# Performance work log

Measured on AMD Instinct MI355X. Metric: run time of the kernel, lower is better.

The kernel has to match this reference:

```python
import jax, jax.numpy as jnp
import numpy as np
import math

G = 8; N0 = 16384; DEG = 8; E = G * N0 * DEG
C = 128; H = 256; OUT = 128; L = 3
RATIO = 0.5; EPS_FA = 0.1


def setup_inputs():
    key = jax.random.key(0)
    ks = jax.random.split(key, 10)
    x = jax.random.normal(ks[0], (G * N0, C), jnp.float32)
    e = jax.random.randint(ks[1], (2, E), 0, N0)
    off = jnp.repeat(jnp.arange(G) * N0, N0 * DEG)  # per-graph node offsets
    edge_index = (e + off[None, :]).astype(jnp.int32)  # (2, E), edges stay within their graph
    batch = jnp.repeat(jnp.arange(G), N0).astype(jnp.int32)
    root = jax.random.normal(ks[2], (G, C), jnp.float32)
    s = 0.05
    att_l = jax.random.normal(ks[3], (L, C), jnp.float32) * s
    att_r = jax.random.normal(ks[4], (L, C), jnp.float32) * s
    w_ih = jax.random.normal(ks[5], (3 * H, C * L), jnp.float32) * s
    w_hh = jax.random.normal(ks[6], (3 * H, H), jnp.float32) * s
    b_ih = jnp.zeros(3 * H, jnp.float32)
    b_hh = jnp.zeros(3 * H, jnp.float32)
    w_fin = jax.random.normal(ks[7], (OUT, H), jnp.float32) * s
    b_fin = jnp.zeros(OUT, jnp.float32)
    w_root = jax.random.normal(ks[8], (OUT, C), jnp.float32) * s
    b_root = jnp.zeros(OUT, jnp.float32)
    residual_alpha = jnp.float32(0.5)
    return dict(x=x, edge_index=edge_index, batch=batch, root=root, att_l=att_l, att_r=att_r,
                w_ih=w_ih, w_hh=w_hh, b_ih=b_ih, b_hh=b_hh, w_fin=w_fin, b_fin=b_fin,
                w_root=w_root, b_root=b_root, residual_alpha=residual_alpha)


def _faconv(xc, x0, src, dst, emask, al_w, ar_w, n):
    # gcn_norm with self-loops: deg over dst (+1 for self loop), w_ij = d_i^-1/2 d_j^-1/2
    deg = jax.ops.segment_sum(emask, dst, num_segments=n) + 1.0
    dinv = jax.lax.rsqrt(deg)
    w = dinv[src] * dinv[dst] * emask
    al = xc @ al_w  # (n,)
    ar = xc @ ar_w
    alpha = jnp.tanh(al[dst] + ar[src])
    out = jax.ops.segment_sum((w * alpha)[:, None] * xc[src], dst, num_segments=n)
    # self-loop message (weight 1/deg_i, alpha = tanh(al_i + ar_i))
    out = out + ((dinv * dinv) * jnp.tanh(al + ar))[:, None] * xc
    return out + EPS_FA * x0


def _forward(x, root, att_l, att_r, w_ih, w_hh, b_ih, b_hh, w_fin, b_fin, w_root, b_root, residual_alpha, edge_index):
    src = edge_index[0]
    dst = edge_index[1]
    emask = jnp.ones(src.shape[0], jnp.float32)  # edge validity mask (replaces dynamic edge filtering)
    cur, orig = x, x
    npg = N0  # nodes per graph at current layer (static)
    outs = []
    for i in range(L):
        n = G * npg
        h = jax.nn.relu(_faconv(cur, orig, src, dst, emask, att_l[i], att_r[i], n))
        outs.append(h.reshape(G, npg, C).max(axis=1))  # global_max_pool per graph
        # ASTGPool: score = out-degree on edge_index[0], per-graph top-k (k = ceil(npg*ratio))
        score = jax.ops.segment_sum(emask, src, num_segments=n)
        k = int(math.ceil(npg * RATIO))
        _, idx = jax.lax.top_k(score.reshape(G, npg), k)
        perm = (idx + (jnp.arange(G) * npg)[:, None]).reshape(-1)  # (G*k,) global kept-node ids
        keep = jnp.zeros(n, bool).at[perm].set(True)
        emask = emask * keep[src].astype(jnp.float32) * keep[dst].astype(jnp.float32)
        nmap = jnp.zeros(n, src.dtype).at[perm].set(jnp.arange(G * k, dtype=src.dtype))
        src, dst = nmap[src], nmap[dst]  # dead edges map to node 0 but have emask==0
        cur, orig, npg = h[perm], orig[perm], k  # multiplier = 1.0
    fused = jnp.concatenate(outs, axis=1)  # (G, C*L)
    # single-step GRU with h0 = 0
    gi = fused @ w_ih.T + b_ih
    ir, iz, inn = jnp.split(gi, 3, axis=1)
    br, bz, bn = jnp.split(b_hh, 3)
    r = jax.nn.sigmoid(ir + br)
    z = jax.nn.sigmoid(iz + bz)
    ncand = jnp.tanh(inn + r * bn)
    hgru = (1.0 - z) * ncand
    gnn_emb = hgru @ w_fin.T + b_fin
    root_emb = root @ w_root.T + b_root
    return residual_alpha * gnn_emb + (1.0 - residual_alpha) * root_emb


def reference(x, edge_index, batch, root, att_l, att_r, w_ih, w_hh, b_ih, b_hh, w_fin, b_fin, w_root, b_root, residual_alpha):
    del batch  # graphs are contiguous equal-size blocks; batch structure is encoded in G, N0
    return _forward(x, root, att_l, att_r, w_ih, w_hh, b_ih, b_hh, w_fin, b_fin, w_root, b_root, residual_alpha, edge_index)
```

## Files before the change

kernel.cpp:

```cpp
#include <hip/hip_runtime.h>
#include <math.h>

#define G 8
#define N0 16384
#define NEDGE (G*N0*8)
#define EPG (NEDGE/G)
#define C 128
#define EPS_FA 0.1f
#define SMAX 2048

typedef unsigned short ushort_t;
typedef unsigned int uint_t;

__device__ inline ushort_t f2bf(float f) {
    uint_t u = __float_as_uint(f);
    uint_t r = (u + 0x7FFFu + ((u >> 16) & 1u)) >> 16;
    return (ushort_t)r;
}
__device__ inline uint_t pack2bf(float a, float b) {
    return (uint_t)f2bf(a) | ((uint_t)f2bf(b) << 16);
}
__device__ inline float bflo(uint_t w) { return __uint_as_float(w << 16); }
__device__ inline float bfhi(uint_t w) { return __uint_as_float(w & 0xFFFF0000u); }

__global__ void __launch_bounds__(256) k_hist0(const int* __restrict__ ei,
                                               unsigned int* __restrict__ bh,
                                               ushort_t* __restrict__ lrank) {
    __shared__ unsigned int h[N0];
    int t = threadIdx.x;
    for (int i = t; i < N0; i += 256) h[i] = 0;
    __syncthreads();
    int base = blockIdx.x * 8192;
    int gbase = (blockIdx.x >> 4) * N0;
    for (int i = t; i < 8192; i += 256) {
        int s = ei[base + i] - gbase;
        int d = ei[NEDGE + base + i] - gbase;
        unsigned int old = atomicAdd(&h[d], 1u);
        lrank[base + i] = (ushort_t)(old & 0xFFFFu);
        atomicAdd(&h[s], 0x10000u);
    }
    __syncthreads();
    unsigned int* o = bh + (size_t)blockIdx.x * N0;
    for (int i = t; i < N0; i += 256) o[i] = h[i];
}

__global__ void k_sumdeg(unsigned int* __restrict__ bh, int* __restrict__ degI,
                         int* __restrict__ score, int shift, int nsub, int n,
                         float* __restrict__ pooled) {
    int i = blockIdx.x * 256 + threadIdx.x;
    if (pooled && i < G * 384) pooled[i] = 0.0f;
    if (i >= n) return;
    int bins = 1 << shift;
    int g = i >> shift, u = i & (bins - 1);
    unsigned int* p = bh + ((size_t)(g * nsub) << shift) + u;
    unsigned int run = 0; int as = 0;
    for (int b = 0; b < nsub; b++) {
        unsigned int w = p[(size_t)b * bins];
        p[(size_t)b * bins] = run;
        run += w & 0xFFFFu; as += (int)(w >> 16);
    }
    degI[i] = (int)run; score[i] = as;
}

__global__ void k_alar(const float* __restrict__ x,
                       const float* __restrict__ attl, const float* __restrict__ attr,
                       float* __restrict__ al, float* __restrict__ ar,
                       ushort_t* __restrict__ xb, int n) {
    int wid  = (blockIdx.x * blockDim.x + threadIdx.x) >> 6;
    int lane = threadIdx.x & 63;
    if (wid >= n) return;
    float2 v  = ((const float2*)(x + (size_t)wid * C))[lane];
    ((uint_t*)(xb + (size_t)wid * C))[lane] = pack2bf(v.x, v.y);
    float2 l2 = ((const float2*)attl)[lane];
    float2 r2 = ((const float2*)attr)[lane];
    float sl = v.x * l2.x + v.y * l2.y;
    float sr = v.x * r2.x + v.y * r2.y;
    for (int o = 32; o >= 1; o >>= 1) { sl += __shfl_xor(sl, o); sr += __shfl_xor(sr, o); }
    if (lane == 0) { al[wid] = sl; ar[wid] = sr; }
}

__global__ void __launch_bounds__(256) k_scan1(const int* __restrict__ degI,
                                               int* __restrict__ rowptr,
                                               int* __restrict__ bsum) {
    __shared__ int part[256];
    int t = threadIdx.x;
    int base = blockIdx.x * 2048 + t * 8;
    int v[8]; int s = 0;
    for (int i = 0; i < 8; i++) { v[i] = degI[base + i]; s += v[i]; }
    part[t] = s; __syncthreads();
    for (int o = 1; o < 256; o <<= 1) {
        int val = part[t];
        int add = (t >= o) ? part[t - o] : 0;
        __syncthreads();
        part[t] = val + add;
        __syncthreads();
    }
    int run = (t == 0) ? 0 : part[t - 1];
    if (t == 255) bsum[blockIdx.x] = part[255];
    for (int i = 0; i < 8; i++) { rowptr[base + i] = run; run += v[i]; }
}

__global__ void k_scan3s(int* __restrict__ rowptr,
                         const int* __restrict__ bsum, const int* __restrict__ degI,
                         const float* __restrict__ al, const float* __restrict__ ar,
                         float* __restrict__ dinv, float* __restrict__ selfco,
                         unsigned char* __restrict__ keep, int* __restrict__ nmap, int n) {
    __shared__ int base_s;
    int t = threadIdx.x;
    if (t < 64) {
        int c = blockIdx.x >> 3;
        int vv = (t < c) ? bsum[t] : 0;
        for (int o = 32; o >= 1; o >>= 1) vv += __shfl_xor(vv, o);
        if (t == 0) base_s = vv;
    }
    __syncthreads();
    int i = blockIdx.x * 256 + t;
    if (i >= n) return;
    rowptr[i] += base_s;
    float d  = (float)degI[i] + 1.0f;
    float di = rsqrtf(d);
    dinv[i]   = di;
    selfco[i] = di * di * tanhf(al[i] + ar[i]);
    keep[i] = 0; nmap[i] = 0;
}

__global__ void k_fill(const int* __restrict__ src, const int* __restrict__ dst,
                       const unsigned char* __restrict__ em,
                       const float* __restrict__ dinv, const float* __restrict__ al,
                       const float* __restrict__ ar,
                       const int* __restrict__ rowptr,
                       const unsigned int* __restrict__ bpre,
                       const ushort_t* __restrict__ lrank,
                       int2* __restrict__ edges,
                       int ebShift, int nsubShift, int binShift) {
    int gph = blockIdx.x & 7;
    int chunk = blockIdx.x >> 3;
    int e = gph * EPG + chunk * 256 + threadIdx.x;
    if (em && !em[e]) return;
    int s = src[e], d = dst[e];
    float cf = dinv[s] * dinv[d] * tanhf(al[d] + ar[s]);
    int b = e >> ebShift;
    int gb = (b >> nsubShift) << binShift;
    int slot = rowptr[d] + (int)bpre[((size_t)b << binShift) + (d - gb)] + (int)lrank[e];
    edges[slot] = make_int2(s, __float_as_int(cf));
}

#define ACC4(W, CF) { a0 += (CF) * bflo((W).x); a1 += (CF) * bfhi((W).x); \
                      a2 += (CF) * bflo((W).y); a3 += (CF) * bfhi((W).y); }
__global__ void __launch_bounds__(256) k_msg_csr(
        const int* __restrict__ rowptr, const int* __restrict__ degI,
        const int2* __restrict__ edges,
        const ushort_t* __restrict__ cur, const ushort_t* __restrict__ xb,
        const int* __restrict__ oidx, const float* __restrict__ selfco,
        ushort_t* __restrict__ h, float* __restrict__ pb, int npg) {
    __shared__ float pm[8 * 128];
    int g    = blockIdx.x & 7;
    int ib   = blockIdx.x >> 3;
    int sub  = threadIdx.x >> 5;
    int lane = threadIdx.x & 31;
    int v = g * npg + ib * 8 + sub;
    int rs = rowptr[v], deg = degI[v];
    int o = oidx ? oidx[v] : v;
    uint2 cw = ((const uint2*)(cur + (size_t)v * C))[lane];
    uint2 xw = ((const uint2*)(xb  + (size_t)o * C))[lane];
    float sc = selfco[v];
    float a0 = 0.0f, a1 = 0.0f, a2 = 0.0f, a3 = 0.0f;
    for (int j0 = 0; j0 < deg; j0 += 32) {
        int cnt = deg - j0; if (cnt > 32) cnt = 32;
        int2 er = make_int2(0, 0);
        if (lane < cnt) er = edges[rs + j0 + lane];
        uint2 w0 = make_uint2(0,0), w1 = w0, w2 = w0, w3 = w0;
        {
            int s0 = __shfl(er.x, 0, 32);
            if (0 < cnt) w0 = ((const uint2*)(cur + (size_t)s0 * C))[lane];
            int s1 = __shfl(er.x, 1, 32);
            if (1 < cnt) w1 = ((const uint2*)(cur + (size_t)s1 * C))[lane];
            int s2 = __shfl(er.x, 2, 32);
            if (2 < cnt) w2 = ((const uint2*)(cur + (size_t)s2 * C))[lane];
            int s3 = __shfl(er.x, 3, 32);
            if (3 < cnt) w3 = ((const uint2*)(cur + (size_t)s3 * C))[lane];
        }
        int j = 0;
        for (; j + 4 <= cnt; j += 4) {
            float cf0 = __int_as_float(__shfl(er.y, j, 32));
            ACC4(w0, cf0);
            int sn0 = __shfl(er.x, j + 4, 32);
            if (j + 4 < cnt) w0 = ((const uint2*)(cur + (size_t)sn0 * C))[lane];
            float cf1 = __int_as_float(__shfl(er.y, j + 1, 32));
            ACC4(w1, cf1);
            int sn1 = __shfl(er.x, j + 5, 32);
            if (j + 5 < cnt) w1 = ((const uint2*)(cur + (size_t)sn1 * C))[lane];
            float cf2 = __int_as_float(__shfl(er.y, j + 2, 32));
            ACC4(w2, cf2);
            int sn2 = __shfl(er.x, j + 6, 32);
            if (j + 6 < cnt) w2 = ((const uint2*)(cur + (size_t)sn2 * C))[lane];
            float cf3 = __int_as_float(__shfl(er.y, j + 3, 32));
            ACC4(w3, cf3);
            int sn3 = __shfl(er.x, j + 7, 32);
            if (j + 7 < cnt) w3 = ((const uint2*)(cur + (size_t)sn3 * C))[lane];
        }
        if (j < cnt)     { float cf = __int_as_float(__shfl(er.y, j,     32)); ACC4(w0, cf); }
        if (j + 1 < cnt) { float cf = __int_as_float(__shfl(er.y, j + 1, 32)); ACC4(w1, cf); }
        if (j + 2 < cnt) { float cf = __int_as_float(__shfl(er.y, j + 2, 32)); ACC4(w2, cf); }
    }
    float r0 = fmaxf(a0 + sc * bflo(cw.x) + EPS_FA * bflo(xw.x), 0.0f);
    float r1 = fmaxf(a1 + sc * bfhi(cw.x) + EPS_FA * bfhi(xw.x), 0.0f);
    float r2 = fmaxf(a2 + sc * bflo(cw.y) + EPS_FA * bflo(xw.y), 0.0f);
    float r3 = fmaxf(a3 + sc * bfhi(cw.y) + EPS_FA * bfhi(xw.y), 0.0f);
    uint2 hw; hw.x = pack2bf(r0, r1); hw.y = pack2bf(r2, r3);
    ((uint2*)(h + (size_t)v * C))[lane] = hw;
    float4 rr = make_float4(r0, r1, r2, r3);
    ((float4*)(pm + sub * 128))[lane] = rr;
    __syncthreads();
    int t = threadIdx.x;
    if (t < 128) {
        float m = pm[t];
        for (int s = 1; s < 8; s++) m = fmaxf(m, pm[s * 128 + t]);
        pb[(size_t)blockIdx.x * 128 + t] = m;
    }
}

__global__ void __launch_bounds__(256) k_poolred(const float* __restrict__ pb,
                                                 float* __restrict__ pooled, int layer) {
    __shared__ float sm[256];
    int g = blockIdx.x & 7;
    int ch = blockIdx.x >> 3;
    int t = threadIdx.x;
    int c = t & 127, half = t >> 7;
    float m = 0.0f;
    for (int i = 0; i < 32; i++) {
        int r = ch * 64 + half * 32 + i;
        m = fmaxf(m, pb[(size_t)(g + 8 * r) * 128 + c]);
    }
    sm[t] = m;
    __syncthreads();
    if (t < 128) {
        float mm = fmaxf(sm[t], sm[t + 128]);
        atomicMax((unsigned int*)&pooled[g * 384 + layer * 128 + c], __float_as_uint(mm));
    }
}

__global__ void __launch_bounds__(256) k_hist(const int* __restrict__ score, int npg, int nb,
                                              int* __restrict__ blockhist) {
    __shared__ int lh[SMAX];
    int g = blockIdx.x / nb, b = blockIdx.x % nb, t = threadIdx.x;
    for (int s = t; s < SMAX; s += 256) lh[s] = 0;
    __syncthreads();
    int s = score[g * npg + b * 256 + t];
    if (s > SMAX - 1) s = SMAX - 1;
    atomicAdd(&lh[s], 1);
    __syncthreads();
    int* outp = blockhist + ((size_t)g * nb + b) * SMAX;
    for (int i = t; i < SMAX; i += 256) outp[i] = lh[i];
}

__global__ void __launch_bounds__(256) k_binprefix(int* __restrict__ blockhist,
                                                   int* __restrict__ hist, int nb) {
    __shared__ int tile[64 * 256];
    int g = blockIdx.x >> 3, ch = blockIdx.x & 7, t = threadIdx.x;
    int s0 = ch * 256;
    int* bg = blockhist + (size_t)g * nb * SMAX + s0;
    for (int b = 0; b < nb; b++) tile[b * 256 + t] = bg[(size_t)b * SMAX + t];
    __syncthreads();
    int acc = 0;
    for (int b = 0; b < nb; b++) {
        int v = tile[b * 256 + t];
        tile[b * 256 + t] = acc;
        acc += v;
    }
    __syncthreads();
    for (int b = 0; b < nb; b++) bg[(size_t)b * SMAX + t] = tile[b * 256 + t];
    hist[g * SMAX + s0 + t] = acc;
}

__global__ void __launch_bounds__(256) k_rank(const int* __restrict__ score,
                                              const int* __restrict__ blockhist,
                                              const int* __restrict__ hist,
                                              int npg, int nb, int k,
                                              unsigned char* __restrict__ keep,
                                              int* __restrict__ nmap, int* __restrict__ perm) {
    __shared__ int bp[SMAX];
    __shared__ int part[256];
    __shared__ int cs[256];
    int g = blockIdx.x / nb, b = blockIdx.x % nb, t = threadIdx.x;
    const int* hg = hist + g * SMAX;
    int v[8]; int sm = 0;
    for (int i = 0; i < 8; i++) { v[i] = hg[SMAX - 1 - (t * 8 + i)]; sm += v[i]; }
    part[t] = sm; __syncthreads();
    for (int o = 1; o < 256; o <<= 1) {
        int val = part[t];
        int add = (t >= o) ? part[t - o] : 0;
        __syncthreads();
        part[t] = val + add;
        __syncthreads();
    }
    int run = (t == 0) ? 0 : part[t - 1];
    for (int i = 0; i < 8; i++) { bp[SMAX - 1 - (t * 8 + i)] = run; run += v[i]; }
    int vv = b * 256 + t;
    int s = score[g * npg + vv];
    if (s > SMAX - 1) s = SMAX - 1;
    cs[t] = s;
    __syncthreads();
    int cnt = 0;
    for (int u = 0; u < t; u++) cnt += (cs[u] == s);
    int pos = bp[s] + blockhist[((size_t)g * nb + b) * SMAX + s] + cnt;
    if (pos < k) {
        int vg = g * npg + vv;
        int nid = g * k + pos;
        keep[vg] = 1; nmap[vg] = nid; perm[nid] = vg;
    }
}

__global__ void k_gather_alar(const ushort_t* __restrict__ h, const int* __restrict__ perm,
                              const int* __restrict__ oidx,
                              const float* __restrict__ attlN, const float* __restrict__ attrN,
                              ushort_t* __restrict__ curN, int* __restrict__ oidxN,
                              float* __restrict__ al, float* __restrict__ ar, int m) {
    int i = blockIdx.x * 256 + threadIdx.x;
    if (i >= m * 32) return;
    int j = i >> 5, c4 = i & 31;
    int p = perm[j];
    uint2 w = ((const uint2*)(h + (size_t)p * C))[c4];
    ((uint2*)(curN + (size_t)j * C))[c4] = w;
    float f0 = bflo(w.x), f1 = bfhi(w.x), f2 = bflo(w.y), f3 = bfhi(w.y);
    float4 l4 = ((const float4*)attlN)[c4];
    float4 r4 = ((const float4*)attrN)[c4];
    float sl = f0 * l4.x + f1 * l4.y + f2 * l4.z + f3 * l4.w;
    float sr = f0 * r4.x + f1 * r4.y + f2 * r4.z + f3 * r4.w;
    for (int o = 16; o >= 1; o >>= 1) { sl += __shfl_xor(sl, o); sr += __shfl_xor(sr, o); }
    if (c4 == 0) {
        al[j] = sl; ar[j] = sr;
        oidxN[j] = oidx ? oidx[p] : p;
    }
}

__global__ void __launch_bounds__(256) k_remap_hist(
        const int* __restrict__ inS, const int* __restrict__ inD,
        const unsigned char* __restrict__ inEm,
        int* __restrict__ src, int* __restrict__ dst, unsigned char* __restrict__ em,
        const unsigned char* __restrict__ keep, const int* __restrict__ nmap,
        unsigned int* __restrict__ bh, ushort_t* __restrict__ lrank, int kN) {
    __shared__ unsigned int h[8192];
    int t = threadIdx.x;
    for (int i = t; i < kN; i += 256) h[i] = 0;
    __syncthreads();
    int base = blockIdx.x * 4096;
    int gb = (blockIdx.x >> 5) * kN;
    for (int i = t; i < 4096; i += 256) {
        int e = base + i;
        int s = inS[e], d = inD[e];
        bool ok = (!inEm || inEm[e]) && keep[s] && keep[d];
        if (ok) {
            int ns = nmap[s], nd = nmap[d];
            src[e] = ns; dst[e] = nd; em[e] = 1;
            unsigned int old = atomicAdd(&h[nd - gb], 1u);
            lrank[e] = (ushort_t)(old & 0xFFFFu);
            atomicAdd(&h[ns - gb], 0x10000u);
        } else { src[e] = 0; dst[e] = 0; em[e] = 0; }
    }
    __syncthreads();
    unsigned int* o = bh + (size_t)blockIdx.x * kN;
    for (int i = t; i < kN; i += 256) o[i] = h[i];
}

__global__ void __launch_bounds__(256) k_gi(const float* __restrict__ pooled,
                                            const float* __restrict__ wih,
                                            const float* __restrict__ bih,
                                            float* __restrict__ gi) {
    int g = blockIdx.y;
    int row = blockIdx.x * 4 + (threadIdx.x >> 6);
    int lane = threadIdx.x & 63;
    const float* w = wih + (size_t)row * 384;
    const float* f = pooled + g * 384;
    float s = 0.0f;
    #pragma unroll
    for (int i = 0; i < 6; i++) s += w[i * 64 + lane] * f[i * 64 + lane];
    for (int o = 32; o >= 1; o >>= 1) s += __shfl_xor(s, o);
    if (lane == 0) gi[g * 768 + row] = s + bih[row];
}

__global__ void __launch_bounds__(256) k_gru_fin(const float* __restrict__ gi,
        const float* __restrict__ bhh, const float* __restrict__ wfin,
        const float* __restrict__ bfin, const float* __restrict__ wroot,
        const float* __restrict__ broot, const float* __restrict__ rootv,
        const float* __restrict__ alphap, float* __restrict__ out) {
    int g = blockIdx.x, t = threadIdx.x;
    __shared__ float hg[256];
    {
        float r  = 1.0f / (1.0f + expf(-(gi[g * 768 + t]       + bhh[t])));
        float z  = 1.0f / (1.0f + expf(-(gi[g * 768 + 256 + t] + bhh[256 + t])));
        float nc = tanhf(gi[g * 768 + 512 + t] + r * bhh[512 + t]);
        hg[t] = (1.0f - z) * nc;
    }
    __syncthreads();
    float a = alphap[0];
    int wv = t >> 6, lane = t & 63;
    const float* rg = rootv + (size_t)g * 128;
    for (int oo = 0; oo < 32; oo++) {
        int o = wv * 32 + oo;
        const float* wf = wfin + (size_t)o * 256;
        float sf = wf[lane] * hg[lane] + wf[64 + lane] * hg[64 + lane]
                 + wf[128 + lane] * hg[128 + lane] + wf[192 + lane] * hg[192 + lane];
        const float* wr = wroot + (size_t)o * 128;
        float sr = wr[lane] * rg[lane] + wr[64 + lane] * rg[64 + lane];
        float s = a * sf + (1.0f - a) * sr;
        for (int sh = 32; sh >= 1; sh >>= 1) s += __shfl_xor(s, sh);
        if (lane == 0)
            out[g * 128 + o] = s + a * bfin[o] + (1.0f - a) * broot[o];
    }
}

extern "C" void kernel_launch(void* const* d_in, const int* in_sizes, int n_in,
                              void* d_out, int out_size, void* d_ws, size_t ws_size,
                              hipStream_t stream) {
    const float* x      = (const float*)d_in[0];
    const int*   ei     = (const int*)d_in[1];
    const float* rootv  = (const float*)d_in[3];
    const float* att_l  = (const float*)d_in[4];
    const float* att_r  = (const float*)d_in[5];
    const float* w_ih   = (const float*)d_in[6];
    const float* b_ih   = (const float*)d_in[8];
    const float* b_hh   = (const float*)d_in[9];
    const float* w_fin  = (const float*)d_in[10];
    const float* b_fin  = (const float*)d_in[11];
    const float* w_root = (const float*)d_in[12];
    const float* b_root = (const float*)d_in[13];
    const float* alphap = (const float*)d_in[14];
    float* out = (float*)d_out;

    char* wsb = (char*)d_ws;
    size_t off = 0;
    auto alloc = [&](size_t bytes) -> char* {
        char* p = wsb + off; off += (bytes + 255) & ~(size_t)255; return p;
    };
    ushort_t* xb   = (ushort_t*)alloc((size_t)131072 * C * 2);
    ushort_t* bufH = (ushort_t*)alloc((size_t)131072 * C * 2);
    ushort_t* bufC = (ushort_t*)alloc((size_t)65536  * C * 2);
    int*   srcA   = (int*)alloc((size_t)NEDGE * 4);
    int*   dstA   = (int*)alloc((size_t)NEDGE * 4);
    unsigned char* emask = (unsigned char*)alloc(NEDGE);
    int2*  edges  = (int2*)alloc((size_t)NEDGE * 8);
    ushort_t* lrank = (ushort_t*)alloc((size_t)NEDGE * 2);
    float* al     = (float*)alloc(131072 * 4);
    float* ar     = (float*)alloc(131072 * 4);
    float* dinv   = (float*)alloc(131072 * 4);
    float* selfco = (float*)alloc(131072 * 4);
    int*   degI   = (int*)alloc(131072 * 4);
    int*   score  = (int*)alloc(131072 * 4);
    int*   rowptr = (int*)alloc(131072 * 4);
    int*   bsum   = (int*)alloc(256 * 4);
    unsigned char* keep = (unsigned char*)alloc(131072);
    int*   nmap   = (int*)alloc(131072 * 4);
    int*   perm   = (int*)alloc(65536 * 4);
    int*   oidxA  = (int*)alloc(65536 * 4);
    int*   oidxB  = (int*)alloc(32768 * 4);
    float* pooled = (float*)alloc(G * 384 * 4);
    float* giBuf  = (float*)alloc(G * 768 * 4);
    int*   blockhist = (int*)alloc((size_t)G * 64 * SMAX * 4);
    int*   histT  = (int*)alloc((size_t)G * SMAX * 4);
    unsigned int* bh = (unsigned int*)alloc((size_t)128 * N0 * 4);
    float* pb = (float*)bh;

    k_hist0<<<128, 256, 0, stream>>>(ei, bh, lrank);
    k_sumdeg<<<131072 / 256, 256, 0, stream>>>(bh, degI, score, 14, 16, 131072, pooled);

    const int ns[3]   = {131072, 65536, 32768};
    const int npgs[3] = {16384, 8192, 4096};
    const int ks[3]   = {8192, 4096, 0};
    const int shifts[3] = {14, 13, 12};

    for (int l = 0; l < 3; l++) {
        int n = ns[l], npg = npgs[l], k = ks[l];
        const ushort_t* cur = (l == 0) ? xb : bufC;
        const int* oidx = (l == 0) ? nullptr : (l == 1 ? oidxA : oidxB);
        int* oidxN = (l == 0) ? oidxA : oidxB;
        const int* eS = (l == 0) ? ei : srcA;
        const int* eD = (l == 0) ? ei + NEDGE : dstA;
        const unsigned char* eM = (l == 0) ? nullptr : emask;
        int ebShift   = (l == 0) ? 13 : 12;
        int nsubShift = (l == 0) ? 4  : 5;
        int binShift  = shifts[l];

        if (l == 0)
            k_alar<<<n / 4, 256, 0, stream>>>(x, att_l, att_r, al, ar, xb, n);

        int nblk = n / 2048;
        k_scan1<<<nblk, 256, 0, stream>>>(degI, rowptr, bsum);
        k_scan3s<<<n / 256, 256, 0, stream>>>(rowptr, bsum, degI, al, ar,
                                              dinv, selfco, keep, nmap, n);

        k_fill<<<NEDGE / 256, 256, 0, stream>>>(eS, eD, eM, dinv, al, ar,
                                                rowptr, bh, lrank, edges,
                                                ebShift, nsubShift, binShift);
        k_msg_csr<<<n / 8, 256, 0, stream>>>(rowptr, degI, edges, cur, xb, oidx,
                                             selfco, bufH, pb, npg);
        k_poolred<<<npg / 64, 256, 0, stream>>>(pb, pooled, l);

        if (l < 2) {
            int nb = npg / 256;
            k_hist<<<G * nb, 256, 0, stream>>>(score, npg, nb, blockhist);
            k_binprefix<<<G * 8, 256, 0, stream>>>(blockhist, histT, nb);
            k_rank<<<G * nb, 256, 0, stream>>>(score, blockhist, histT, npg, nb, k,
                                               keep, nmap, perm);
            int m = G * k;
            k_gather_alar<<<(m * 32 + 255) / 256, 256, 0, stream>>>(
                bufH, perm, oidx, att_l + (l + 1) * C, att_r + (l + 1) * C,
                bufC, oidxN, al, ar, m);
            k_remap_hist<<<256, 256, 0, stream>>>(eS, eD, eM, srcA, dstA, emask,
                                                  keep, nmap, bh, lrank, k);
            k_sumdeg<<<(G * k + 255) / 256, 256, 0, stream>>>(bh, degI, score,
                                                              shifts[l + 1], 32, G * k,
                                                              nullptr);
        }
    }

    k_gi<<<dim3(192, G), 256, 0, stream>>>(pooled, w_ih, b_ih, giBuf);
    k_gru_fin<<<G, 256, 0, stream>>>(giBuf, b_hh, w_fin, b_fin, w_root, b_root,
                                     rootv, alphap, out);
}
```

Before: 438.9 us.

## Merge independent kernels into combined launches to cut launch count

Pairs independent kernels that previously ran back to back: sumdeg with alar, fill with score histogram, message passing with bin prefix, pool reduction with rank, and gather with edge remap. Each combined launch splits its blocks by blockIdx range into the two roles. This removes several kernel launches and serialisation bubbles per layer, letting small kernels overlap with larger ones. The bin-prefix role is also retiled from 8 chunks of 256 to 32 chunks of 64, and merging raises shared-memory use in the combined kernels, which may lower occupancy for the heavy message kernel.

```diff
diff --git a/kernel.cpp b/kernel.cpp
--- a/kernel.cpp
+++ b/kernel.cpp
@@ -44,11 +44,41 @@
     for (int i = t; i < N0; i += 256) o[i] = h[i];
 }
 
+__global__ void __launch_bounds__(256) k_sumdeg_alar(
+        unsigned int* __restrict__ bh, int* __restrict__ degI, int* __restrict__ score,
+        float* __restrict__ pooled,
+        const float* __restrict__ x, const float* __restrict__ attl,
+        const float* __restrict__ attr, float* __restrict__ al, float* __restrict__ ar,
+        ushort_t* __restrict__ xb) {
+    int t = threadIdx.x;
+    if ((int)blockIdx.x < 512) {
+        int i = blockIdx.x * 256 + t;
+        if (i < G * 384) pooled[i] = 0.0f;
+        unsigned int* p = bh + ((size_t)((i >> 14) * 16) << 14) + (i & 16383);
+        unsigned int run = 0; int as = 0;
+        for (int b = 0; b < 16; b++) {
+            unsigned int w = p[(size_t)b << 14];
+            p[(size_t)b << 14] = run;
+            run += w & 0xFFFFu; as += (int)(w >> 16);
+        }
+        degI[i] = (int)run; score[i] = as;
+    } else {
+        int idx = (blockIdx.x - 512) * 256 + t;
+        int wid = idx >> 6, lane = idx & 63;
+        float2 v  = ((const float2*)(x + (size_t)wid * C))[lane];
+        ((uint_t*)(xb + (size_t)wid * C))[lane] = pack2bf(v.x, v.y);
+        float2 l2 = ((const float2*)attl)[lane];
+        float2 r2 = ((const float2*)attr)[lane];
+        float sl = v.x * l2.x + v.y * l2.y;
+        float sr = v.x * r2.x + v.y * r2.y;
+        for (int o = 32; o >= 1; o >>= 1) { sl += __shfl_xor(sl, o); sr += __shfl_xor(sr, o); }
+        if (lane == 0) { al[wid] = sl; ar[wid] = sr; }
+    }
+}
+
 __global__ void k_sumdeg(unsigned int* __restrict__ bh, int* __restrict__ degI,
-                         int* __restrict__ score, int shift, int nsub, int n,
-                         float* __restrict__ pooled) {
+                         int* __restrict__ score, int shift, int nsub, int n) {
     int i = blockIdx.x * 256 + threadIdx.x;
-    if (pooled && i < G * 384) pooled[i] = 0.0f;
     if (i >= n) return;
     int bins = 1 << shift;
     int g = i >> shift, u = i & (bins - 1);
@@ -62,23 +92,6 @@
     degI[i] = (int)run; score[i] = as;
 }
 
-__global__ void k_alar(const float* __restrict__ x,
-                       const float* __restrict__ attl, const float* __restrict__ attr,
-                       float* __restrict__ al, float* __restrict__ ar,
-                       ushort_t* __restrict__ xb, int n) {
-    int wid  = (blockIdx.x * blockDim.x + threadIdx.x) >> 6;
-    int lane = threadIdx.x & 63;
-    if (wid >= n) return;
-    float2 v  = ((const float2*)(x + (size_t)wid * C))[lane];
-    ((uint_t*)(xb + (size_t)wid * C))[lane] = pack2bf(v.x, v.y);
-    float2 l2 = ((const float2*)attl)[lane];
-    float2 r2 = ((const float2*)attr)[lane];
-    float sl = v.x * l2.x + v.y * l2.y;
-    float sr = v.x * r2.x + v.y * r2.y;
-    for (int o = 32; o >= 1; o >>= 1) { sl += __shfl_xor(sl, o); sr += __shfl_xor(sr, o); }
-    if (lane == 0) { al[wid] = sl; ar[wid] = sr; }
-}
-
 __global__ void __launch_bounds__(256) k_scan1(const int* __restrict__ degI,
                                                int* __restrict__ rowptr,
                                                int* __restrict__ bsum) {
@@ -124,40 +137,80 @@
     keep[i] = 0; nmap[i] = 0;
 }
 
-__global__ void k_fill(const int* __restrict__ src, const int* __restrict__ dst,
-                       const unsigned char* __restrict__ em,
-                       const float* __restrict__ dinv, const float* __restrict__ al,
-                       const float* __restrict__ ar,
-                       const int* __restrict__ rowptr,
-                       const unsigned int* __restrict__ bpre,
-                       const ushort_t* __restrict__ lrank,
-                       int2* __restrict__ edges,
-                       int ebShift, int nsubShift, int binShift) {
-    int gph = blockIdx.x & 7;
-    int chunk = blockIdx.x >> 3;
-    int e = gph * EPG + chunk * 256 + threadIdx.x;
-    if (em && !em[e]) return;
-    int s = src[e], d = dst[e];
-    float cf = dinv[s] * dinv[d] * tanhf(al[d] + ar[s]);
-    int b = e >> ebShift;
-    int gb = (b >> nsubShift) << binShift;
-    int slot = rowptr[d] + (int)bpre[((size_t)b << binShift) + (d - gb)] + (int)lrank[e];
-    edges[slot] = make_int2(s, __float_as_int(cf));
+__global__ void __launch_bounds__(256) k_fill_hist(
+        const int* __restrict__ src, const int* __restrict__ dst,
+        const unsigned char* __restrict__ em,
+        const float* __restrict__ dinv, const float* __restrict__ al,
+        const float* __restrict__ ar,
+        const int* __restrict__ rowptr, const unsigned int* __restrict__ bpre,
+        const ushort_t* __restrict__ lrank, int2* __restrict__ edges,
+        int ebShift, int nsubShift, int binShift,
+        const int* __restrict__ score, int npg, int nb,
+        int* __restrict__ blockhist, int histBlocks) {
+    __shared__ int lh[SMAX];
+    int t = threadIdx.x;
+    if ((int)blockIdx.x < histBlocks) {
+        int g = blockIdx.x / nb, b = blockIdx.x % nb;
+        for (int s = t; s < SMAX; s += 256) lh[s] = 0;
+        __syncthreads();
+        int s = score[g * npg + b * 256 + t];
+        if (s > SMAX - 1) s = SMAX - 1;
+        atomicAdd(&lh[s], 1);
+        __syncthreads();
+        int* outp = blockhist + ((size_t)g * nb + b) * SMAX;
+        for (int i = t; i < SMAX; i += 256) outp[i] = lh[i];
+    } else {
+        int fb = blockIdx.x - histBlocks;
+        int gph = fb & 7, chunk = fb >> 3;
+        int e = gph * EPG + chunk * 256 + t;
+        if (em && !em[e]) return;
+        int s = src[e], d = dst[e];
+        float cf = dinv[s] * dinv[d] * tanhf(al[d] + ar[s]);
+        int b = e >> ebShift;
+        int gb = (b >> nsubShift) << binShift;
+        int slot = rowptr[d] + (int)bpre[((size_t)b << binShift) + (d - gb)] + (int)lrank[e];
+        edges[slot] = make_int2(s, __float_as_int(cf));
+    }
 }
 
 #define ACC4(W, CF) { a0 += (CF) * bflo((W).x); a1 += (CF) * bfhi((W).x); \
                       a2 += (CF) * bflo((W).y); a3 += (CF) * bfhi((W).y); }
-__global__ void __launch_bounds__(256) k_msg_csr(
+__global__ void __launch_bounds__(256) k_msg_bp(
         const int* __restrict__ rowptr, const int* __restrict__ degI,
         const int2* __restrict__ edges,
         const ushort_t* __restrict__ cur, const ushort_t* __restrict__ xb,
         const int* __restrict__ oidx, const float* __restrict__ selfco,
-        ushort_t* __restrict__ h, float* __restrict__ pb, int npg) {
+        ushort_t* __restrict__ h, float* __restrict__ pb, int npg,
+        int* __restrict__ blockhist, int* __restrict__ histT, int nb, int bpBlocks) {
     __shared__ float pm[8 * 128];
-    int g    = blockIdx.x & 7;
-    int ib   = blockIdx.x >> 3;
-    int sub  = threadIdx.x >> 5;
-    int lane = threadIdx.x & 31;
+    __shared__ int tile[4096];
+    int t = threadIdx.x;
+    if ((int)blockIdx.x < bpBlocks) {
+        int g = blockIdx.x >> 5, ch = blockIdx.x & 31;
+        int s0 = ch * 64;
+        int* bg = blockhist + (size_t)g * nb * SMAX;
+        int tot = nb * 64;
+        for (int i = t; i < tot; i += 256)
+            tile[i] = bg[(size_t)(i >> 6) * SMAX + s0 + (i & 63)];
+        __syncthreads();
+        if (t < 64) {
+            int acc = 0;
+            for (int b = 0; b < nb; b++) {
+                int idx = b * 64 + t;
+                int v = tile[idx]; tile[idx] = acc; acc += v;
+            }
+            histT[g * SMAX + s0 + t] = acc;
+        }
+        __syncthreads();
+        for (int i = t; i < tot; i += 256)
+            bg[(size_t)(i >> 6) * SMAX + s0 + (i & 63)] = tile[i];
+        return;
+    }
+    int mb   = blockIdx.x - bpBlocks;
+    int g    = mb & 7;
+    int ib   = mb >> 3;
+    int sub  = t >> 5;
+    int lane = t & 31;
     int v = g * npg + ib * 8 + sub;
     int rs = rowptr[v], deg = degI[v];
     int o = oidx ? oidx[v] : v;
@@ -212,155 +265,120 @@
     float4 rr = make_float4(r0, r1, r2, r3);
     ((float4*)(pm + sub * 128))[lane] = rr;
     __syncthreads();
-    int t = threadIdx.x;
     if (t < 128) {
         float m = pm[t];
         for (int s = 1; s < 8; s++) m = fmaxf(m, pm[s * 128 + t]);
-        pb[(size_t)blockIdx.x * 128 + t] = m;
-    }
-}
-
-__global__ void __launch_bounds__(256) k_poolred(const float* __restrict__ pb,
-                                                 float* __restrict__ pooled, int layer) {
-    __shared__ float sm[256];
-    int g = blockIdx.x & 7;
-    int ch = blockIdx.x >> 3;
-    int t = threadIdx.x;
-    int c = t & 127, half = t >> 7;
-    float m = 0.0f;
-    for (int i = 0; i < 32; i++) {
-        int r = ch * 64 + half * 32 + i;
-        m = fmaxf(m, pb[(size_t)(g + 8 * r) * 128 + c]);
-    }
-    sm[t] = m;
-    __syncthreads();
-    if (t < 128) {
-        float mm = fmaxf(sm[t], sm[t + 128]);
-        atomicMax((unsigned int*)&pooled[g * 384 + layer * 128 + c], __float_as_uint(mm));
-    }
-}
-
-__global__ void __launch_bounds__(256) k_hist(const int* __restrict__ score, int npg, int nb,
-                                              int* __restrict__ blockhist) {
-    __shared__ int lh[SMAX];
-    int g = blockIdx.x / nb, b = blockIdx.x % nb, t = threadIdx.x;
-    for (int s = t; s < SMAX; s += 256) lh[s] = 0;
-    __syncthreads();
-    int s = score[g * npg + b * 256 + t];
-    if (s > SMAX - 1) s = SMAX - 1;
-    atomicAdd(&lh[s], 1);
-    __syncthreads();
-    int* outp = blockhist + ((size_t)g * nb + b) * SMAX;
-    for (int i = t; i < SMAX; i += 256) outp[i] = lh[i];
-}
-
-__global__ void __launch_bounds__(256) k_binprefix(int* __restrict__ blockhist,
-                                                   int* __restrict__ hist, int nb) {
-    __shared__ int tile[64 * 256];
-    int g = blockIdx.x >> 3, ch = blockIdx.x & 7, t = threadIdx.x;
-    int s0 = ch * 256;
-    int* bg = blockhist + (size_t)g * nb * SMAX + s0;
-    for (int b = 0; b < nb; b++) tile[b * 256 + t] = bg[(size_t)b * SMAX + t];
-    __syncthreads();
-    int acc = 0;
-    for (int b = 0; b < nb; b++) {
-        int v = tile[b * 256 + t];
-        tile[b * 256 + t] = acc;
-        acc += v;
-    }
-    __syncthreads();
-    for (int b = 0; b < nb; b++) bg[(size_t)b * SMAX + t] = tile[b * 256 + t];
-    hist[g * SMAX + s0 + t] = acc;
-}
-
-__global__ void __launch_bounds__(256) k_rank(const int* __restrict__ score,
-                                              const int* __restrict__ blockhist,
-                                              const int* __restrict__ hist,
-                                              int npg, int nb, int k,
-                                              unsigned char* __restrict__ keep,
-                                              int* __restrict__ nmap, int* __restrict__ perm) {
+        pb[(size_t)mb * 128 + t] = m;
+    }
+}
+
+__global__ void __launch_bounds__(256) k_pool_rank(
+        const float* __restrict__ pb, float* __restrict__ pooled, int layer,
+        const int* __restrict__ score, const int* __restrict__ blockhist,
+        const int* __restrict__ hist, int npg, int nb, int k,
+        unsigned char* __restrict__ keep, int* __restrict__ nmap,
+        int* __restrict__ perm, int rankBlocks) {
     __shared__ int bp[SMAX];
     __shared__ int part[256];
     __shared__ int cs[256];
-    int g = blockIdx.x / nb, b = blockIdx.x % nb, t = threadIdx.x;
-    const int* hg = hist + g * SMAX;
-    int v[8]; int sm = 0;
-    for (int i = 0; i < 8; i++) { v[i] = hg[SMAX - 1 - (t * 8 + i)]; sm += v[i]; }
-    part[t] = sm; __syncthreads();
-    for (int o = 1; o < 256; o <<= 1) {
-        int val = part[t];
-        int add = (t >= o) ? part[t - o] : 0;
-        __syncthreads();
-        part[t] = val + add;
-        __syncthreads();
-    }
-    int run = (t == 0) ? 0 : part[t - 1];
-    for (int i = 0; i < 8; i++) { bp[SMAX - 1 - (t * 8 + i)] = run; run += v[i]; }
-    int vv = b * 256 + t;
-    int s = score[g * npg + vv];
-    if (s > SMAX - 1) s = SMAX - 1;
-    cs[t] = s;
-    __syncthreads();
-    int cnt = 0;
-    for (int u = 0; u < t; u++) cnt += (cs[u] == s);
-    int pos = bp[s] + blockhist[((size_t)g * nb + b) * SMAX + s] + cnt;
-    if (pos < k) {
-        int vg = g * npg + vv;
-        int nid = g * k + pos;
-        keep[vg] = 1; nmap[vg] = nid; perm[nid] = vg;
-    }
-}
-
-__global__ void k_gather_alar(const ushort_t* __restrict__ h, const int* __restrict__ perm,
-                              const int* __restrict__ oidx,
-                              const float* __restrict__ attlN, const float* __restrict__ attrN,
-                              ushort_t* __restrict__ curN, int* __restrict__ oidxN,
-                              float* __restrict__ al, float* __restrict__ ar, int m) {
-    int i = blockIdx.x * 256 + threadIdx.x;
-    if (i >= m * 32) return;
-    int j = i >> 5, c4 = i & 31;
-    int p = perm[j];
-    uint2 w = ((const uint2*)(h + (size_t)p * C))[c4];
-    ((uint2*)(curN + (size_t)j * C))[c4] = w;
-    float f0 = bflo(w.x), f1 = bfhi(w.x), f2 = bflo(w.y), f3 = bfhi(w.y);
-    float4 l4 = ((const float4*)attlN)[c4];
-    float4 r4 = ((const float4*)attrN)[c4];
-    float sl = f0 * l4.x + f1 * l4.y + f2 * l4.z + f3 * l4.w;
-    float sr = f0 * r4.x + f1 * r4.y + f2 * r4.z + f3 * r4.w;
-    for (int o = 16; o >= 1; o >>= 1) { sl += __shfl_xor(sl, o); sr += __shfl_xor(sr, o); }
-    if (c4 == 0) {
-        al[j] = sl; ar[j] = sr;
-        oidxN[j] = oidx ? oidx[p] : p;
-    }
-}
-
-__global__ void __launch_bounds__(256) k_remap_hist(
+    __shared__ float sm[256];
+    int t = threadIdx.x;
+    if ((int)blockIdx.x < rankBlocks) {
+        int g = blockIdx.x / nb, b = blockIdx.x % nb;
+        const int* hg = hist + g * SMAX;
+        int v[8]; int smv = 0;
+        for (int i = 0; i < 8; i++) { v[i] = hg[SMAX - 1 - (t * 8 + i)]; smv += v[i]; }
+        part[t] = smv; __syncthreads();
+        for (int o = 1; o < 256; o <<= 1) {
+            int val = part[t];
+            int add = (t >= o) ? part[t - o] : 0;
+            __syncthreads();
+            part[t] = val + add;
+            __syncthreads();
+        }
+        int run = (t == 0) ? 0 : part[t - 1];
+        for (int i = 0; i < 8; i++) { bp[SMAX - 1 - (t * 8 + i)] = run; run += v[i]; }
+        int vv = b * 256 + t;
+        int s = score[g * npg + vv];
+        if (s > SMAX - 1) s = SMAX - 1;
+        cs[t] = s;
+        __syncthreads();
+        int cnt = 0;
+        for (int u = 0; u < t; u++) cnt += (cs[u] == s);
+        int pos = bp[s] + blockhist[((size_t)g * nb + b) * SMAX + s] + cnt;
+        if (pos < k) {
+            int vg = g * npg + vv;
+            int nid = g * k + pos;
+            keep[vg] = 1; nmap[vg] = nid; perm[nid] = vg;
+        }
+    } else {
+        int pr = blockIdx.x - rankBlocks;
+        int g = pr & 7, ch = pr >> 3;
+        int c = t & 127, half = t >> 7;
+        float m = 0.0f;
+        for (int i = 0; i < 32; i++) {
+            int r = ch * 64 + half * 32 + i;
+            m = fmaxf(m, pb[(size_t)(g + 8 * r) * 128 + c]);
+        }
+        sm[t] = m;
+        __syncthreads();
+        if (t < 128) {
+            float mm = fmaxf(sm[t], sm[t + 128]);
+            atomicMax((unsigned int*)&pooled[g * 384 + layer * 128 + c], __float_as_uint(mm));
+        }
+    }
+}
+
+__global__ void __launch_bounds__(256) k_gather_remap(
+        const ushort_t* __restrict__ h, const int* __restrict__ perm,
+        const int* __restrict__ oidx,
+        const float* __restrict__ attlN, const float* __restrict__ attrN,
+        ushort_t* __restrict__ curN, int* __restrict__ oidxN,
+        float* __restrict__ al, float* __restrict__ ar, int m,
         const int* __restrict__ inS, const int* __restrict__ inD,
         const unsigned char* __restrict__ inEm,
         int* __restrict__ src, int* __restrict__ dst, unsigned char* __restrict__ em,
         const unsigned char* __restrict__ keep, const int* __restrict__ nmap,
         unsigned int* __restrict__ bh, ushort_t* __restrict__ lrank, int kN) {
-    __shared__ unsigned int h[8192];
-    int t = threadIdx.x;
-    for (int i = t; i < kN; i += 256) h[i] = 0;
-    __syncthreads();
-    int base = blockIdx.x * 4096;
-    int gb = (blockIdx.x >> 5) * kN;
-    for (int i = t; i < 4096; i += 256) {
-        int e = base + i;
-        int s = inS[e], d = inD[e];
-        bool ok = (!inEm || inEm[e]) && keep[s] && keep[d];
-        if (ok) {
-            int ns = nmap[s], nd = nmap[d];
-            src[e] = ns; dst[e] = nd; em[e] = 1;
-            unsigned int old = atomicAdd(&h[nd - gb], 1u);
-            lrank[e] = (ushort_t)(old & 0xFFFFu);
-            atomicAdd(&h[ns - gb], 0x10000u);
-        } else { src[e] = 0; dst[e] = 0; em[e] = 0; }
-    }
-    __syncthreads();
-    unsigned int* o = bh + (size_t)blockIdx.x * kN;
-    for (int i = t; i < kN; i += 256) o[i] = h[i];
+    __shared__ unsigned int hh[8192];
+    int t = threadIdx.x;
+    if ((int)blockIdx.x < 256) {
+        for (int i = t; i < kN; i += 256) hh[i] = 0;
+        __syncthreads();
+        int base = blockIdx.x * 4096;
+        int gb = (blockIdx.x >> 5) * kN;
+        for (int i = t; i < 4096; i += 256) {
+            int e = base + i;
+            int s = inS[e], d = inD[e];
+            bool ok = (!inEm || inEm[e]) && keep[s] && keep[d];
+            if (ok) {
+                int ns = nmap[s], nd = nmap[d];
+                src[e] = ns; dst[e] = nd; em[e] = 1;
+                unsigned int old = atomicAdd(&hh[nd - gb], 1u);
+                lrank[e] = (ushort_t)(old & 0xFFFFu);
+                atomicAdd(&hh[ns - gb], 0x10000u);
+            } else { src[e] = 0; dst[e] = 0; em[e] = 0; }
+        }
+        __syncthreads();
+        unsigned int* o = bh + (size_t)blockIdx.x * kN;
+        for (int i = t; i < kN; i += 256) o[i] = hh[i];
+    } else {
+        int i = (blockIdx.x - 256) * 256 + t;
+        int j = i >> 5, c4 = i & 31;
+        int p = perm[j];
+        uint2 w = ((const uint2*)(h + (size_t)p * C))[c4];
+        ((uint2*)(curN + (size_t)j * C))[c4] = w;
+        float f0 = bflo(w.x), f1 = bfhi(w.x), f2 = bflo(w.y), f3 = bfhi(w.y);
+        float4 l4 = ((const float4*)attlN)[c4];
+        float4 r4 = ((const float4*)attrN)[c4];
+        float sl = f0 * l4.x + f1 * l4.y + f2 * l4.z + f3 * l4.w;
+        float sr = f0 * r4.x + f1 * r4.y + f2 * r4.z + f3 * r4.w;
+        for (int o = 16; o >= 1; o >>= 1) { sl += __shfl_xor(sl, o); sr += __shfl_xor(sr, o); }
+        if (c4 == 0) {
+            al[j] = sl; ar[j] = sr;
+            oidxN[j] = oidx ? oidx[p] : p;
+        }
+    }
 }
 
 __global__ void __launch_bounds__(256) k_gi(const float* __restrict__ pooled,
@@ -462,7 +480,8 @@
     float* pb = (float*)bh;
 
     k_hist0<<<128, 256, 0, stream>>>(ei, bh, lrank);
-    k_sumdeg<<<131072 / 256, 256, 0, stream>>>(bh, degI, score, 14, 16, 131072, pooled);
+    k_sumdeg_alar<<<512 + 32768, 256, 0, stream>>>(bh, degI, score, pooled,
+                                                   x, att_l, att_r, al, ar, xb);
 
     const int ns[3]   = {131072, 65536, 32768};
     const int npgs[3] = {16384, 8192, 4096};
@@ -480,37 +499,35 @@
         int ebShift   = (l == 0) ? 13 : 12;
         int nsubShift = (l == 0) ? 4  : 5;
         int binShift  = shifts[l];
-
-        if (l == 0)
-            k_alar<<<n / 4, 256, 0, stream>>>(x, att_l, att_r, al, ar, xb, n);
-
-        int nblk = n / 2048;
-        k_scan1<<<nblk, 256, 0, stream>>>(degI, rowptr, bsum);
+        int nb = npg / 256;
+
+        k_scan1<<<n / 2048, 256, 0, stream>>>(degI, rowptr, bsum);
         k_scan3s<<<n / 256, 256, 0, stream>>>(rowptr, bsum, degI, al, ar,
                                               dinv, selfco, keep, nmap, n);
 
-        k_fill<<<NEDGE / 256, 256, 0, stream>>>(eS, eD, eM, dinv, al, ar,
-                                                rowptr, bh, lrank, edges,
-                                                ebShift, nsubShift, binShift);
-        k_msg_csr<<<n / 8, 256, 0, stream>>>(rowptr, degI, edges, cur, xb, oidx,
-                                             selfco, bufH, pb, npg);
-        k_poolred<<<npg / 64, 256, 0, stream>>>(pb, pooled, l);
+        int histBlocks = (l < 2) ? G * nb : 0;
+        k_fill_hist<<<histBlocks + NEDGE / 256, 256, 0, stream>>>(
+            eS, eD, eM, dinv, al, ar, rowptr, bh, lrank, edges,
+            ebShift, nsubShift, binShift, score, npg, nb, blockhist, histBlocks);
+
+        int bpBlocks = (l < 2) ? 256 : 0;
+        k_msg_bp<<<bpBlocks + n / 8, 256, 0, stream>>>(
+            rowptr, degI, edges, cur, xb, oidx, selfco, bufH, pb, npg,
+            blockhist, histT, nb, bpBlocks);
+
+        int rankBlocks = (l < 2) ? G * nb : 0;
+        k_pool_rank<<<rankBlocks + npg / 64, 256, 0, stream>>>(
+            pb, pooled, l, score, blockhist, histT, npg, nb, k,
+            keep, nmap, perm, rankBlocks);
 
         if (l < 2) {
-            int nb = npg / 256;
-            k_hist<<<G * nb, 256, 0, stream>>>(score, npg, nb, blockhist);
-            k_binprefix<<<G * 8, 256, 0, stream>>>(blockhist, histT, nb);
-            k_rank<<<G * nb, 256, 0, stream>>>(score, blockhist, histT, npg, nb, k,
-                                               keep, nmap, perm);
             int m = G * k;
-            k_gather_alar<<<(m * 32 + 255) / 256, 256, 0, stream>>>(
+            k_gather_remap<<<256 + m / 8, 256, 0, stream>>>(
                 bufH, perm, oidx, att_l + (l + 1) * C, att_r + (l + 1) * C,
-                bufC, oidxN, al, ar, m);
-            k_remap_hist<<<256, 256, 0, stream>>>(eS, eD, eM, srcA, dstA, emask,
-                                                  keep, nmap, bh, lrank, k);
+                bufC, oidxN, al, ar, m,
+                eS, eD, eM, srcA, dstA, emask, keep, nmap, bh, lrank, k);
             k_sumdeg<<<(G * k + 255) / 256, 256, 0, stream>>>(bh, degI, score,
-                                                              shifts[l + 1], 32, G * k,
-                                                              nullptr);
+                                                              shifts[l + 1], 32, G * k);
         }
     }
 
```

Result: faster. 402.8 us (-8.2%).
